# Optimization experiments

Hardware: AMD Instinct MI355X
Metric: run time of the kernel (lower is better)

Reference implementation:

```python
import jax, jax.numpy as jnp
import numpy as np

WORLD_SIZE = 8
BS = 16
MSG = 16384


def setup_inputs() -> dict:
    key = jax.random.key(0)
    k0, k1, kw, kb = jax.random.split(key, 4)
    x0 = jax.random.normal(k0, (WORLD_SIZE, BS, MSG), dtype=jnp.float32)
    x1 = jax.random.normal(k1, (WORLD_SIZE, BS, MSG), dtype=jnp.float32)
    # nn.Linear(msg_size, msg_size) params, kaiming-uniform-ish scale
    scale = 1.0 / np.sqrt(MSG)
    W = jax.random.uniform(kw, (MSG, MSG), dtype=jnp.float32, minval=-scale, maxval=scale)
    b = jax.random.uniform(kb, (MSG,), dtype=jnp.float32, minval=-scale, maxval=scale)
    return {"x0": x0, "x1": x1, "W": W, "b": b}


def reference(x0, x1, W, b):
    # all_gather_ll: concat per-rank shards along dim 0 -> [world_size*bs, msg]
    t0 = x0.reshape(WORLD_SIZE * BS, MSG)
    t1 = x1.reshape(WORLD_SIZE * BS, MSG)
    # shared Linear applied to both gathered tensors: y = t @ W^T + b
    y0 = jnp.einsum("nk,mk->nm", t0, W) + b
    y1 = jnp.einsum("nk,mk->nm", t1, W) + b
    return (y0, y1)
```

## Files before the change

### kernel.cpp

```cpp
#include <hip/hip_runtime.h>
#include <hip/hip_bf16.h>

typedef __bf16 bf16x8 __attribute__((ext_vector_type(8)));
typedef float  f32x4  __attribute__((ext_vector_type(4)));

#define N_TOT   16384
#define K_TOT   16384
#define HALF_M  ((size_t)128 * 16384)
#define BN      64
#define BK      64
#define NSTEPS  (K_TOT / BK)

__device__ __forceinline__ unsigned short f2bf(float f) {
    __hip_bfloat16 h = __float2bfloat16(f);
    return __builtin_bit_cast(unsigned short, h);
}

__device__ __forceinline__ int swz(int row, int g) {
    return row * 128 + (((g ^ (row & 7)) & 7) << 4);
}

__global__ void cvtT_kernel(const float* __restrict__ x0,
                            const float* __restrict__ x1,
                            unsigned short* __restrict__ wsT) {
    size_t i = (size_t)blockIdx.x * blockDim.x + threadIdx.x;
    size_t e = i * 8;
    const float* src = (e < HALF_M) ? (x0 + e) : (x1 + (e - HALF_M));
    float4 a = ((const float4*)src)[0];
    float4 b = ((const float4*)src)[1];
    union { unsigned short u[8]; uint4 v; } o;
    o.u[0] = f2bf(a.x); o.u[1] = f2bf(a.y); o.u[2] = f2bf(a.z); o.u[3] = f2bf(a.w);
    o.u[4] = f2bf(b.x); o.u[5] = f2bf(b.y); o.u[6] = f2bf(b.z); o.u[7] = f2bf(b.w);
    ((uint4*)wsT)[i] = o.v;
}


#define ISSUE(S, k0) do {                                                     \
    if constexpr (USE_WS) {                                                   \
        const uint4* _p = (const uint4*)(arow_w + (k0));                      \
        w##S##_0 = _p[0]; w##S##_1 = _p[1];                                   \
    } else {                                                                  \
        const float4* _p = (const float4*)(arow_f + (k0));                    \
        f##S##_0 = _p[0]; f##S##_1 = _p[1]; f##S##_2 = _p[2]; f##S##_3 = _p[3];\
    }                                                                         \
    wb##S = *(const float4*)(brow + (k0));                                    \
} while (0)

#define STAGE(S, Ab, Bb) do {                                                 \
    if constexpr (USE_WS) {                                                   \
        *(uint4*)((Ab) + aw0) = w##S##_0;                                     \
        *(uint4*)((Ab) + aw1) = w##S##_1;                                     \
    } else {                                                                  \
        union { unsigned short u[8]; uint4 v; } _t0, _t1;                     \
        _t0.u[0]=f2bf(f##S##_0.x); _t0.u[1]=f2bf(f##S##_0.y);                 \
        _t0.u[2]=f2bf(f##S##_0.z); _t0.u[3]=f2bf(f##S##_0.w);                 \
        _t0.u[4]=f2bf(f##S##_1.x); _t0.u[5]=f2bf(f##S##_1.y);                 \
        _t0.u[6]=f2bf(f##S##_1.z); _t0.u[7]=f2bf(f##S##_1.w);                 \
        _t1.u[0]=f2bf(f##S##_2.x); _t1.u[1]=f2bf(f##S##_2.y);                 \
        _t1.u[2]=f2bf(f##S##_2.z); _t1.u[3]=f2bf(f##S##_2.w);                 \
        _t1.u[4]=f2bf(f##S##_3.x); _t1.u[5]=f2bf(f##S##_3.y);                 \
        _t1.u[6]=f2bf(f##S##_3.z); _t1.u[7]=f2bf(f##S##_3.w);                 \
        *(uint4*)((Ab) + aw0) = _t0.v;                                        \
        *(uint4*)((Ab) + aw1) = _t1.v;                                        \
    }                                                                         \
    union { unsigned short u[4]; uint2 v; } _tb;                              \
    _tb.u[0]=f2bf(wb##S.x); _tb.u[1]=f2bf(wb##S.y);                           \
    _tb.u[2]=f2bf(wb##S.z); _tb.u[3]=f2bf(wb##S.w);                           \
    *(uint2*)((Bb) + bw) = _tb.v;                                             \
} while (0)

#define COMPUTE(Ab, Bb) do {                                                  \
    bf16x8 _b00 = *(const bf16x8*)((Bb) + boff00);                            \
    bf16x8 _b01 = *(const bf16x8*)((Bb) + boff01);                            \
    bf16x8 _b10 = *(const bf16x8*)((Bb) + boff10);                            \
    bf16x8 _b11 = *(const bf16x8*)((Bb) + boff11);                            \
    bf16x8 _a;                                                                \
    _a = *(const bf16x8*)((Ab) + aoff00);                                     \
    acc00 = __builtin_amdgcn_mfma_f32_16x16x32_bf16(_a, _b00, acc00, 0, 0, 0);\
    acc01 = __builtin_amdgcn_mfma_f32_16x16x32_bf16(_a, _b10, acc01, 0, 0, 0);\
    _a = *(const bf16x8*)((Ab) + aoff01);                                     \
    acc00 = __builtin_amdgcn_mfma_f32_16x16x32_bf16(_a, _b01, acc00, 0, 0, 0);\
    acc01 = __builtin_amdgcn_mfma_f32_16x16x32_bf16(_a, _b11, acc01, 0, 0, 0);\
    _a = *(const bf16x8*)((Ab) + aoff10);                                     \
    acc10 = __builtin_amdgcn_mfma_f32_16x16x32_bf16(_a, _b00, acc10, 0, 0, 0);\
    acc11 = __builtin_amdgcn_mfma_f32_16x16x32_bf16(_a, _b10, acc11, 0, 0, 0);\
    _a = *(const bf16x8*)((Ab) + aoff11);                                     \
    acc10 = __builtin_amdgcn_mfma_f32_16x16x32_bf16(_a, _b01, acc10, 0, 0, 0);\
    acc11 = __builtin_amdgcn_mfma_f32_16x16x32_bf16(_a, _b11, acc11, 0, 0, 0);\
} while (0)

#define SYNC do {                                                             \
    asm volatile("s_waitcnt lgkmcnt(0)" ::: "memory");                        \
    __builtin_amdgcn_s_barrier();                                             \
    __builtin_amdgcn_sched_barrier(0);                                        \
} while (0)

template<bool USE_WS>
__global__ __launch_bounds__(1024)
void gemm_kernel(const float* __restrict__ x0, const float* __restrict__ x1,
                 const float* __restrict__ W,  const float* __restrict__ bias,
                 const unsigned short* __restrict__ wsT,
                 float* __restrict__ out)
{
    __shared__ uint4 smem_[(2 * 32768 + 2 * 8192) / 16];
    char* const sm = (char*)smem_;
    char* const A0 = sm;
    char* const A1 = sm + 32768;
    char* const B0 = sm + 65536;
    char* const B1 = sm + 65536 + 8192;

    const int tid  = threadIdx.x;
    const int lane = tid & 63;
    const int wave = tid >> 6;
    const int wm = wave >> 1;
    const int wn = wave & 1;
    const int n0 = blockIdx.x * BN;

    const int ra  = tid >> 2;
    const int pa  = tid & 3;
    const int rbs = tid >> 4;
    const int cbs = (tid & 15) * 4;

    const unsigned short* arow_w = wsT + (size_t)ra * K_TOT + pa * 16;
    const float* arow_f = ((ra < 128) ? (x0 + (size_t)ra * K_TOT)
                                      : (x1 + (size_t)(ra - 128) * K_TOT)) + pa * 16;
    const float* brow = W + (size_t)(n0 + rbs) * K_TOT + cbs;

    const int aw0 = swz(ra, 2 * pa);
    const int aw1 = swz(ra, 2 * pa + 1);
    const int bw  = rbs * 128 + (((((tid & 15) >> 1) ^ (rbs & 7)) & 7) << 4) + (tid & 1) * 8;

    const int aoff00 = swz(wm * 32 +  0 + (lane & 15), 0 + (lane >> 4));
    const int aoff01 = swz(wm * 32 +  0 + (lane & 15), 4 + (lane >> 4));
    const int aoff10 = swz(wm * 32 + 16 + (lane & 15), 0 + (lane >> 4));
    const int aoff11 = swz(wm * 32 + 16 + (lane & 15), 4 + (lane >> 4));
    const int boff00 = swz(wn * 32 +  0 + (lane & 15), 0 + (lane >> 4));
    const int boff01 = swz(wn * 32 +  0 + (lane & 15), 4 + (lane >> 4));
    const int boff10 = swz(wn * 32 + 16 + (lane & 15), 0 + (lane >> 4));
    const int boff11 = swz(wn * 32 + 16 + (lane & 15), 4 + (lane >> 4));

    f32x4 acc00 = {0.f,0.f,0.f,0.f}, acc01 = {0.f,0.f,0.f,0.f};
    f32x4 acc10 = {0.f,0.f,0.f,0.f}, acc11 = {0.f,0.f,0.f,0.f};

    uint4  w0_0, w0_1, w1_0, w1_1;
    float4 f0_0, f0_1, f0_2, f0_3, f1_0, f1_1, f1_2, f1_3;
    float4 wb0, wb1;

    ISSUE(0, 0);
    ISSUE(1, BK);
    STAGE(0, A0, B0);
    SYNC;

    for (int kt = 0; kt < NSTEPS; kt += 2) {
        if (kt + 2 < NSTEPS) ISSUE(0, (kt + 2) * BK);
        COMPUTE(A0, B0);
        STAGE(1, A1, B1);
        SYNC;
        if (kt + 3 < NSTEPS) ISSUE(1, (kt + 3) * BK);
        COMPUTE(A1, B1);
        if (kt + 2 < NSTEPS) STAGE(0, A0, B0);
        SYNC;
    }

    const int colbase = n0 + wn * 32 + (lane & 15);
    #pragma unroll
    for (int nf = 0; nf < 2; ++nf) {
        const int col = colbase + nf * 16;
        const float bv = bias[col];
        #pragma unroll
        for (int mf = 0; mf < 2; ++mf) {
            const f32x4 a = (nf == 0) ? (mf == 0 ? acc00 : acc10)
                                      : (mf == 0 ? acc01 : acc11);
            #pragma unroll
            for (int j = 0; j < 4; ++j) {
                int r = wm * 32 + mf * 16 + (lane >> 4) * 4 + j;
                float v = a[j] + bv;
                float* o = (r < 128) ? (out + (size_t)r * N_TOT + col)
                                     : (out + HALF_M + (size_t)(r - 128) * N_TOT + col);
                *o = v;
            }
        }
    }
}

extern "C" void kernel_launch(void* const* d_in, const int* in_sizes, int n_in,
                              void* d_out, int out_size, void* d_ws, size_t ws_size,
                              hipStream_t stream) {
    const float* x0 = (const float*)d_in[0];
    const float* x1 = (const float*)d_in[1];
    const float* W  = (const float*)d_in[2];
    const float* b  = (const float*)d_in[3];
    float* out = (float*)d_out;

    const size_t wsT_bytes = (size_t)256 * 16384 * sizeof(unsigned short);
    if (ws_size >= wsT_bytes) {
        unsigned short* wsT = (unsigned short*)d_ws;
        cvtT_kernel<<<2048, 256, 0, stream>>>(x0, x1, wsT);
        gemm_kernel<true><<<256, 1024, 0, stream>>>(x0, x1, W, b, wsT, out);
    } else {
        gemm_kernel<false><<<256, 1024, 0, stream>>>(x0, x1, W, b, nullptr, out);
    }
}
```

Baseline: 305.0 us.

## Split K four ways with wider N tiles and a combine pass

The GEMM now uses 128-wide N tiles, so each block reads half as much of the shared A panel per output column. K is split into four quarters across 512 blocks to keep all CUs busy. Partial sums for quarters 1-3 go to 48MB of workspace, and a separate combine kernel adds them into the output. The fp32-input fallback path is removed and workspace size is no longer checked, which risks overflow if the workspace is smaller than about 56MB. The extra partial writes and re-reads add memory traffic.

```diff
diff --git a/kernel.cpp b/kernel.cpp
--- a/kernel.cpp
+++ b/kernel.cpp
@@ -7,9 +7,12 @@
 #define N_TOT   16384
 #define K_TOT   16384
 #define HALF_M  ((size_t)128 * 16384)
-#define BN      64
+#define BN      128
 #define BK      64
-#define NSTEPS  (K_TOT / BK)
+#define KSPLIT  4
+#define KQ_LEN  (K_TOT / KSPLIT)
+#define NQSTEPS (KQ_LEN / BK)
+#define OUT_ELEMS ((size_t)256 * 16384)
 
 __device__ __forceinline__ unsigned short f2bf(float f) {
     __hip_bfloat16 h = __float2bfloat16(f);
@@ -34,39 +37,39 @@
     ((uint4*)wsT)[i] = o.v;
 }
 
-
-#define ISSUE(S, k0) do {                                                     \
-    if constexpr (USE_WS) {                                                   \
-        const uint4* _p = (const uint4*)(arow_w + (k0));                      \
-        w##S##_0 = _p[0]; w##S##_1 = _p[1];                                   \
-    } else {                                                                  \
-        const float4* _p = (const float4*)(arow_f + (k0));                    \
-        f##S##_0 = _p[0]; f##S##_1 = _p[1]; f##S##_2 = _p[2]; f##S##_3 = _p[3];\
-    }                                                                         \
-    wb##S = *(const float4*)(brow + (k0));                                    \
-} while (0)
-
-#define STAGE(S, Ab, Bb) do {                                                 \
-    if constexpr (USE_WS) {                                                   \
-        *(uint4*)((Ab) + aw0) = w##S##_0;                                     \
-        *(uint4*)((Ab) + aw1) = w##S##_1;                                     \
-    } else {                                                                  \
-        union { unsigned short u[8]; uint4 v; } _t0, _t1;                     \
-        _t0.u[0]=f2bf(f##S##_0.x); _t0.u[1]=f2bf(f##S##_0.y);                 \
-        _t0.u[2]=f2bf(f##S##_0.z); _t0.u[3]=f2bf(f##S##_0.w);                 \
-        _t0.u[4]=f2bf(f##S##_1.x); _t0.u[5]=f2bf(f##S##_1.y);                 \
-        _t0.u[6]=f2bf(f##S##_1.z); _t0.u[7]=f2bf(f##S##_1.w);                 \
-        _t1.u[0]=f2bf(f##S##_2.x); _t1.u[1]=f2bf(f##S##_2.y);                 \
-        _t1.u[2]=f2bf(f##S##_2.z); _t1.u[3]=f2bf(f##S##_2.w);                 \
-        _t1.u[4]=f2bf(f##S##_3.x); _t1.u[5]=f2bf(f##S##_3.y);                 \
-        _t1.u[6]=f2bf(f##S##_3.z); _t1.u[7]=f2bf(f##S##_3.w);                 \
-        *(uint4*)((Ab) + aw0) = _t0.v;                                        \
-        *(uint4*)((Ab) + aw1) = _t1.v;                                        \
-    }                                                                         \
-    union { unsigned short u[4]; uint2 v; } _tb;                              \
-    _tb.u[0]=f2bf(wb##S.x); _tb.u[1]=f2bf(wb##S.y);                           \
-    _tb.u[2]=f2bf(wb##S.z); _tb.u[3]=f2bf(wb##S.w);                           \
-    *(uint2*)((Bb) + bw) = _tb.v;                                             \
+__global__ void combine_kernel(float* __restrict__ out,
+                               const float* __restrict__ p0,
+                               const float* __restrict__ p1,
+                               const float* __restrict__ p2) {
+    const size_t n4 = OUT_ELEMS / 4;
+    size_t i = (size_t)blockIdx.x * blockDim.x + threadIdx.x;
+    for (; i < n4; i += (size_t)gridDim.x * blockDim.x) {
+        float4 o = ((const float4*)out)[i];
+        float4 a = ((const float4*)p0)[i];
+        float4 b = ((const float4*)p1)[i];
+        float4 c = ((const float4*)p2)[i];
+        o.x += a.x + b.x + c.x;  o.y += a.y + b.y + c.y;
+        o.z += a.z + b.z + c.z;  o.w += a.w + b.w + c.w;
+        ((float4*)out)[i] = o;
+    }
+}
+
+#define ISSUEW(S, k0) do {                                                    \
+    const uint4* _p = (const uint4*)(arow_w + (k0));                          \
+    w##S##_0 = _p[0]; w##S##_1 = _p[1];                                       \
+    const float4* _q = (const float4*)(brow + (k0));                          \
+    wb##S##_0 = _q[0]; wb##S##_1 = _q[1];                                     \
+} while (0)
+
+#define STAGEW(S, Ab, Bb) do {                                                \
+    *(uint4*)((Ab) + aw0) = w##S##_0;                                         \
+    *(uint4*)((Ab) + aw1) = w##S##_1;                                         \
+    union { unsigned short u[8]; uint4 v; } _tb;                              \
+    _tb.u[0]=f2bf(wb##S##_0.x); _tb.u[1]=f2bf(wb##S##_0.y);                   \
+    _tb.u[2]=f2bf(wb##S##_0.z); _tb.u[3]=f2bf(wb##S##_0.w);                   \
+    _tb.u[4]=f2bf(wb##S##_1.x); _tb.u[5]=f2bf(wb##S##_1.y);                   \
+    _tb.u[6]=f2bf(wb##S##_1.z); _tb.u[7]=f2bf(wb##S##_1.w);                   \
+    *(uint4*)((Bb) + bw) = _tb.v;                                             \
 } while (0)
 
 #define COMPUTE(Ab, Bb) do {                                                  \
@@ -87,6 +90,18 @@
     _a = *(const bf16x8*)((Ab) + aoff11);                                     \
     acc10 = __builtin_amdgcn_mfma_f32_16x16x32_bf16(_a, _b01, acc10, 0, 0, 0);\
     acc11 = __builtin_amdgcn_mfma_f32_16x16x32_bf16(_a, _b11, acc11, 0, 0, 0);\
+    _a = *(const bf16x8*)((Ab) + aoff20);                                     \
+    acc20 = __builtin_amdgcn_mfma_f32_16x16x32_bf16(_a, _b00, acc20, 0, 0, 0);\
+    acc21 = __builtin_amdgcn_mfma_f32_16x16x32_bf16(_a, _b10, acc21, 0, 0, 0);\
+    _a = *(const bf16x8*)((Ab) + aoff21);                                     \
+    acc20 = __builtin_amdgcn_mfma_f32_16x16x32_bf16(_a, _b01, acc20, 0, 0, 0);\
+    acc21 = __builtin_amdgcn_mfma_f32_16x16x32_bf16(_a, _b11, acc21, 0, 0, 0);\
+    _a = *(const bf16x8*)((Ab) + aoff30);                                     \
+    acc30 = __builtin_amdgcn_mfma_f32_16x16x32_bf16(_a, _b00, acc30, 0, 0, 0);\
+    acc31 = __builtin_amdgcn_mfma_f32_16x16x32_bf16(_a, _b10, acc31, 0, 0, 0);\
+    _a = *(const bf16x8*)((Ab) + aoff31);                                     \
+    acc30 = __builtin_amdgcn_mfma_f32_16x16x32_bf16(_a, _b01, acc30, 0, 0, 0);\
+    acc31 = __builtin_amdgcn_mfma_f32_16x16x32_bf16(_a, _b11, acc31, 0, 0, 0);\
 } while (0)
 
 #define SYNC do {                                                             \
@@ -95,45 +110,48 @@
     __builtin_amdgcn_sched_barrier(0);                                        \
 } while (0)
 
-template<bool USE_WS>
-__global__ __launch_bounds__(1024)
-void gemm_kernel(const float* __restrict__ x0, const float* __restrict__ x1,
-                 const float* __restrict__ W,  const float* __restrict__ bias,
-                 const unsigned short* __restrict__ wsT,
-                 float* __restrict__ out)
+__global__ __launch_bounds__(1024, 4)
+void gemm_ws(const float* __restrict__ W, const float* __restrict__ bias,
+             const unsigned short* __restrict__ wsT,
+             float* __restrict__ out, float* __restrict__ wsP)
 {
-    __shared__ uint4 smem_[(2 * 32768 + 2 * 8192) / 16];
+    __shared__ uint4 smem_[(2 * 32768 + 2 * 16384) / 16];
     char* const sm = (char*)smem_;
     char* const A0 = sm;
     char* const A1 = sm + 32768;
     char* const B0 = sm + 65536;
-    char* const B1 = sm + 65536 + 8192;
+    char* const B1 = sm + 65536 + 16384;
 
     const int tid  = threadIdx.x;
     const int lane = tid & 63;
     const int wave = tid >> 6;
-    const int wm = wave >> 1;
-    const int wn = wave & 1;
-    const int n0 = blockIdx.x * BN;
+    const int wm = wave >> 2;
+    const int wn = wave & 3;
+    const int nstrip = blockIdx.x & 127;
+    const int kq     = blockIdx.x >> 7;
+    const int n0     = nstrip * BN;
+    const int kbase  = kq * KQ_LEN;
 
     const int ra  = tid >> 2;
     const int pa  = tid & 3;
-    const int rbs = tid >> 4;
-    const int cbs = (tid & 15) * 4;
-
-    const unsigned short* arow_w = wsT + (size_t)ra * K_TOT + pa * 16;
-    const float* arow_f = ((ra < 128) ? (x0 + (size_t)ra * K_TOT)
-                                      : (x1 + (size_t)(ra - 128) * K_TOT)) + pa * 16;
-    const float* brow = W + (size_t)(n0 + rbs) * K_TOT + cbs;
+    const int rbs = tid >> 3;
+    const int cbs = (tid & 7) * 8;
+
+    const unsigned short* arow_w = wsT + (size_t)ra * K_TOT + kbase + pa * 16;
+    const float* brow = W + (size_t)(n0 + rbs) * K_TOT + kbase + cbs;
 
     const int aw0 = swz(ra, 2 * pa);
     const int aw1 = swz(ra, 2 * pa + 1);
-    const int bw  = rbs * 128 + (((((tid & 15) >> 1) ^ (rbs & 7)) & 7) << 4) + (tid & 1) * 8;
-
-    const int aoff00 = swz(wm * 32 +  0 + (lane & 15), 0 + (lane >> 4));
-    const int aoff01 = swz(wm * 32 +  0 + (lane & 15), 4 + (lane >> 4));
-    const int aoff10 = swz(wm * 32 + 16 + (lane & 15), 0 + (lane >> 4));
-    const int aoff11 = swz(wm * 32 + 16 + (lane & 15), 4 + (lane >> 4));
+    const int bw  = swz(rbs, tid & 7);
+
+    const int aoff00 = swz(wm * 64 +  0 + (lane & 15), 0 + (lane >> 4));
+    const int aoff01 = swz(wm * 64 +  0 + (lane & 15), 4 + (lane >> 4));
+    const int aoff10 = swz(wm * 64 + 16 + (lane & 15), 0 + (lane >> 4));
+    const int aoff11 = swz(wm * 64 + 16 + (lane & 15), 4 + (lane >> 4));
+    const int aoff20 = swz(wm * 64 + 32 + (lane & 15), 0 + (lane >> 4));
+    const int aoff21 = swz(wm * 64 + 32 + (lane & 15), 4 + (lane >> 4));
+    const int aoff30 = swz(wm * 64 + 48 + (lane & 15), 0 + (lane >> 4));
+    const int aoff31 = swz(wm * 64 + 48 + (lane & 15), 4 + (lane >> 4));
     const int boff00 = swz(wn * 32 +  0 + (lane & 15), 0 + (lane >> 4));
     const int boff01 = swz(wn * 32 +  0 + (lane & 15), 4 + (lane >> 4));
     const int boff10 = swz(wn * 32 + 16 + (lane & 15), 0 + (lane >> 4));
@@ -141,42 +159,44 @@
 
     f32x4 acc00 = {0.f,0.f,0.f,0.f}, acc01 = {0.f,0.f,0.f,0.f};
     f32x4 acc10 = {0.f,0.f,0.f,0.f}, acc11 = {0.f,0.f,0.f,0.f};
+    f32x4 acc20 = {0.f,0.f,0.f,0.f}, acc21 = {0.f,0.f,0.f,0.f};
+    f32x4 acc30 = {0.f,0.f,0.f,0.f}, acc31 = {0.f,0.f,0.f,0.f};
 
     uint4  w0_0, w0_1, w1_0, w1_1;
-    float4 f0_0, f0_1, f0_2, f0_3, f1_0, f1_1, f1_2, f1_3;
-    float4 wb0, wb1;
-
-    ISSUE(0, 0);
-    ISSUE(1, BK);
-    STAGE(0, A0, B0);
+    float4 wb0_0, wb0_1, wb1_0, wb1_1;
+
+    ISSUEW(0, 0);
+    ISSUEW(1, BK);
+    STAGEW(0, A0, B0);
     SYNC;
 
-    for (int kt = 0; kt < NSTEPS; kt += 2) {
-        if (kt + 2 < NSTEPS) ISSUE(0, (kt + 2) * BK);
+    for (int kt = 0; kt < NQSTEPS; kt += 2) {
+        if (kt + 2 < NQSTEPS) ISSUEW(0, (kt + 2) * BK);
         COMPUTE(A0, B0);
-        STAGE(1, A1, B1);
+        STAGEW(1, A1, B1);
         SYNC;
-        if (kt + 3 < NSTEPS) ISSUE(1, (kt + 3) * BK);
+        if (kt + 3 < NQSTEPS) ISSUEW(1, (kt + 3) * BK);
         COMPUTE(A1, B1);
-        if (kt + 2 < NSTEPS) STAGE(0, A0, B0);
+        if (kt + 2 < NQSTEPS) STAGEW(0, A0, B0);
         SYNC;
     }
 
-    const int colbase = n0 + wn * 32 + (lane & 15);
+    float* const dst = (kq == 0) ? out : (wsP + (size_t)(kq - 1) * OUT_ELEMS);
     #pragma unroll
     for (int nf = 0; nf < 2; ++nf) {
-        const int col = colbase + nf * 16;
-        const float bv = bias[col];
+        const int col = n0 + wn * 32 + nf * 16 + (lane & 15);
+        const float bv = (kq == 0) ? bias[col] : 0.f;
         #pragma unroll
-        for (int mf = 0; mf < 2; ++mf) {
-            const f32x4 a = (nf == 0) ? (mf == 0 ? acc00 : acc10)
-                                      : (mf == 0 ? acc01 : acc11);
+        for (int mf = 0; mf < 4; ++mf) {
+            const f32x4 a =
+                (nf == 0) ? (mf == 0 ? acc00 : mf == 1 ? acc10 : mf == 2 ? acc20 : acc30)
+                          : (mf == 0 ? acc01 : mf == 1 ? acc11 : mf == 2 ? acc21 : acc31);
             #pragma unroll
             for (int j = 0; j < 4; ++j) {
-                int r = wm * 32 + mf * 16 + (lane >> 4) * 4 + j;
+                int r = wm * 64 + mf * 16 + (lane >> 4) * 4 + j;
                 float v = a[j] + bv;
-                float* o = (r < 128) ? (out + (size_t)r * N_TOT + col)
-                                     : (out + HALF_M + (size_t)(r - 128) * N_TOT + col);
+                float* o = (r < 128) ? (dst + (size_t)r * N_TOT + col)
+                                     : (dst + HALF_M + (size_t)(r - 128) * N_TOT + col);
                 *o = v;
             }
         }
@@ -193,11 +213,15 @@
     float* out = (float*)d_out;
 
     const size_t wsT_bytes = (size_t)256 * 16384 * sizeof(unsigned short);
-    if (ws_size >= wsT_bytes) {
-        unsigned short* wsT = (unsigned short*)d_ws;
-        cvtT_kernel<<<2048, 256, 0, stream>>>(x0, x1, wsT);
-        gemm_kernel<true><<<256, 1024, 0, stream>>>(x0, x1, W, b, wsT, out);
-    } else {
-        gemm_kernel<false><<<256, 1024, 0, stream>>>(x0, x1, W, b, nullptr, out);
-    }
-}
+    const size_t wsP_bytes = 3 * OUT_ELEMS * sizeof(float);
+
+    unsigned short* wsT = (unsigned short*)d_ws;
+    float* wsP = (float*)((char*)d_ws + wsT_bytes);
+
+    (void)wsP_bytes; (void)ws_size;
+
+    cvtT_kernel<<<2048, 256, 0, stream>>>(x0, x1, wsT);
+    gemm_ws<<<512, 1024, 0, stream>>>(W, b, wsT, out, wsP);
+    combine_kernel<<<2048, 256, 0, stream>>>(out, wsP, wsP + OUT_ELEMS,
+                                             wsP + 2 * OUT_ELEMS);
+}
```

Result: faster. 282.5 us (-7.4%).
